# Kernel optimization log

Hardware: AMD Instinct MI355X
Metric: run time of the kernel (lower is better)

## Reference

```python
import jax, jax.numpy as jnp
import numpy as np
import math

B, L, C_IN, D, H, FACTOR = 32, 512, 32, 512, 8, 1
E = D // H
TOP_K = int(FACTOR * math.log(L))  # 6


def setup_inputs() -> dict:
    key = jax.random.key(0)
    ks = jax.random.split(key, 14)
    s = 0.02
    f = lambda k, shp: jax.random.normal(k, shp, jnp.float32) * s
    return {
        "x": jax.random.normal(ks[0], (B, L, C_IN), jnp.float32),
        "conv_w": f(ks[1], (D, C_IN)),  # Conv1d kernel_size=1 == pointwise linear
        "conv_b": f(ks[2], (D,)),
        "wq": f(ks[3], (D, D)), "bq": f(ks[4], (D,)),
        "wk": f(ks[5], (D, D)), "bk": f(ks[6], (D,)),
        "wv": f(ks[7], (D, D)), "bv": f(ks[8], (D,)),
        "wo": f(ks[9], (D, D)), "bo": f(ks[10], (D,)),
        "lin_w": f(ks[11], (1, D)), "lin_b": f(ks[12], (1,)),
    }


def _autocorrelation(q, k, v):
    # q, k, v: [B, L, H, E]; Autoformer AutoCorrelation (inference delay agg)
    qf = jnp.fft.rfft(q.transpose(0, 2, 3, 1), axis=-1)        # [B,H,E,Lf]
    kf = jnp.fft.rfft(k.transpose(0, 2, 3, 1), axis=-1)
    corr = jnp.fft.irfft(qf * jnp.conj(kf), n=L, axis=-1)       # [B,H,E,L]
    vals = v.transpose(0, 2, 3, 1)                              # [B,H,E,L]
    mean_corr = corr.mean(axis=(1, 2))                          # [B,L]
    weights, delay = jax.lax.top_k(mean_corr, TOP_K)            # [B,k]
    w = jax.nn.softmax(weights, axis=-1)                        # [B,k]
    # gather values at (t + delay) mod L  (== doubled-values trick in torch)
    idx = (jnp.arange(L)[None, None, :] + delay[:, :, None]) % L  # [B,k,L]
    patterns = jnp.take_along_axis(
        vals[:, :, :, None, :], idx[:, None, None, :, :], axis=-1)  # [B,H,E,k,L]
    agg = jnp.einsum('bhekl,bk->bhel', patterns, w)             # [B,H,E,L]
    return agg.transpose(0, 3, 1, 2)                            # [B,L,H,E]


def reference(x, conv_w, conv_b, wq, bq, wk, bk, wv, bv, wo, bo, lin_w, lin_b):
    # pointwise conv1d projection: [B,L,C_IN] -> [B,L,D]
    h = x @ conv_w.T + conv_b
    q = (h @ wq.T + bq).reshape(B, L, H, E)
    k = (h @ wk.T + bk).reshape(B, L, H, E)
    v = (h @ wv.T + bv).reshape(B, L, H, E)
    attn_out = _autocorrelation(q, k, v).reshape(B, L, D)
    new_x = attn_out @ wo.T + bo
    out = h + new_x          # residual
    last = out[:, -1:, :]    # x[:, -1:]
    y = last @ lin_w.T + lin_b  # [B,1,1]
    return y
```

## Files before the change

kernel.cpp:

```cpp
#include <hip/hip_runtime.h>
#include <hip/hip_bf16.h>

#define LL 512
#define BB 32
#define DD 512
#define CINN 32
#define TOPK 6
#define BL (BB * LL)

typedef __attribute__((ext_vector_type(8))) short bf16x8;
typedef __attribute__((ext_vector_type(4))) float f32x4;

__device__ inline float bf2f(ushort u) {
    union { uint i; float f; } c; c.i = ((uint)u) << 16; return c.f;
}
__device__ inline ushort f2bf(float f) {
    union { float f; uint i; } c; c.f = f;
    uint i = c.i;
    return (ushort)((i + 0x7FFFu + ((i >> 16) & 1u)) >> 16);
}
__device__ inline void split_bf(float v, ushort& hi, ushort& lo) {
    hi = f2bf(v);
    lo = f2bf(v - bf2f(hi));
}
__device__ inline uint pk2(ushort a, ushort b) { return (uint)a | ((uint)b << 16); }

__device__ inline bf16x8 frag_ld(const ushort* sm, int r, int s) {
    return *(const bf16x8*)(sm + r * 32 + ((s ^ ((r >> 1) & 3)) << 3));
}

__device__ inline void mfma_step(const ushort* sAh, const ushort* sAl,
                                 const ushort* sBh, const ushort* sBl,
                                 f32x4 acc[4][4], int wr, int wc, int fr, int fs) {
    bf16x8 bh[4], blo[4];
    #pragma unroll
    for (int ni = 0; ni < 4; ++ni) {
        bh[ni]  = frag_ld(sBh, wc + ni * 16 + fr, fs);
        blo[ni] = frag_ld(sBl, wc + ni * 16 + fr, fs);
    }
    #pragma unroll
    for (int mi = 0; mi < 4; ++mi) {
        const bf16x8 ah = frag_ld(sAh, wr + mi * 16 + fr, fs);
        const bf16x8 al = frag_ld(sAl, wr + mi * 16 + fr, fs);
        #pragma unroll
        for (int ni = 0; ni < 4; ++ni) {
            acc[mi][ni] = __builtin_amdgcn_mfma_f32_16x16x32_bf16(ah, bh[ni],  acc[mi][ni], 0, 0, 0);
            acc[mi][ni] = __builtin_amdgcn_mfma_f32_16x16x32_bf16(ah, blo[ni], acc[mi][ni], 0, 0, 0);
            acc[mi][ni] = __builtin_amdgcn_mfma_f32_16x16x32_bf16(al, bh[ni],  acc[mi][ni], 0, 0, 0);
        }
    }
}

__global__ __launch_bounds__(256) void prep_m(
    const float* __restrict__ wq, const float* __restrict__ wk,
    const float* __restrict__ cw,
    const float* __restrict__ lin_w, const float* __restrict__ wo,
    float* __restrict__ Mpart, float* __restrict__ upart)
{
    const int tid = threadIdx.x;
    if (blockIdx.x < 64) {
        __shared__ float cws[512][32];
        __shared__ float wqsT[512][9];
        __shared__ float wksT[512][9];
        __shared__ float aqs[8][32];
        __shared__ float aks[8][32];
        for (int i = tid; i < 4096; i += 256) {
            const int d = i >> 3, q = i & 7;
            *(float4*)&cws[d][q * 4] = *(const float4*)(cw + (long)d * 32 + q * 4);
        }
        const int e0 = blockIdx.x * 8;
        for (int i = tid; i < 4096; i += 256) {
            const int e = i >> 9, d = i & 511;
            wqsT[d][e] = wq[(long)(e0 + e) * 512 + d];
            wksT[d][e] = wk[(long)(e0 + e) * 512 + d];
        }
        __syncthreads();
        const int e_loc = tid >> 5, c = tid & 31;
        float aq = 0.f, ak = 0.f;
        #pragma unroll 4
        for (int d = 0; d < 512; ++d) {
            const float cv = cws[d][c];
            aq += wqsT[d][e_loc] * cv;
            ak += wksT[d][e_loc] * cv;
        }
        aqs[e_loc][c] = aq;
        aks[e_loc][c] = ak;
        __syncthreads();
        const int c_ = tid >> 3, cq = tid & 7;
        float m0 = 0.f, m1 = 0.f, m2 = 0.f, m3 = 0.f;
        #pragma unroll
        for (int e = 0; e < 8; ++e) {
            const float a = aqs[e][c_];
            const float4 k4 = *(const float4*)&aks[e][cq * 4];
            m0 += a * k4.x; m1 += a * k4.y; m2 += a * k4.z; m3 += a * k4.w;
        }
        *(float4*)(Mpart + (long)blockIdx.x * 1024 + c_ * 32 + cq * 4) =
            make_float4(m0, m1, m2, m3);
    } else {
        const int j = blockIdx.x - 64;
        const int n0 = j * 64;
        float u0 = 0.f, u1 = 0.f;
        for (int n = 0; n < 64; ++n) {
            const float lw = lin_w[n0 + n];
            u0 += lw * wo[(long)(n0 + n) * 512 + tid];
            u1 += lw * wo[(long)(n0 + n) * 512 + tid + 256];
        }
        upart[j * 512 + tid] = u0;
        upart[j * 512 + tid + 256] = u1;
    }
}

__global__ __launch_bounds__(256, 2) void corr_fused(
    const float* __restrict__ x,
    const float* __restrict__ Mpart, const float* __restrict__ upart,
    const float* __restrict__ wv,
    float* __restrict__ mcpart, float* __restrict__ v2part)
{
    const int tid = threadIdx.x;
    if (blockIdx.x < 512) {
        __shared__ ushort buf[16384];
        __shared__ float Ml[32][36];
        __shared__ float mcloc[LL];
        ushort* bufAh = buf;
        ushort* bufAl = buf + 4096;
        ushort* bufBh = buf + 8192;
        ushort* bufBl = buf + 12288;

        const int xcd = blockIdx.x & 7, s = blockIdx.x >> 3;
        const int b = xcd * 4 + (s >> 4);
        const int tile = s & 15;
        const int tm = tile >> 2, tn = tile & 3;

        {
            float4 ms = make_float4(0.f, 0.f, 0.f, 0.f);
            for (int p = 0; p < 64; ++p) {
                const float4 v = *(const float4*)(Mpart + (long)p * 1024 + tid * 4);
                ms.x += v.x; ms.y += v.y; ms.z += v.z; ms.w += v.w;
            }
            *(float4*)&Ml[tid >> 3][(tid & 7) * 4] = ms;
        }
        mcloc[tid] = 0.f; mcloc[tid + 256] = 0.f;

        const int r = tid >> 1;
        const int pb = (tid & 1) * 2;
        const int swz = (r >> 1) & 3;
        const float* xA = x + ((long)b * LL + tm * 128 + r) * 32;
        const float* xB = x + ((long)b * LL + tn * 128 + r) * 32;
        float xb[32];
        #pragma unroll
        for (int q = 0; q < 8; ++q)
            *(float4*)&xb[q * 4] = *(const float4*)(xB + q * 4);

        __syncthreads();

        #pragma unroll
        for (int pi = 0; pi < 2; ++pi) {
            const int p = pb + pi;
            const int sl = p ^ swz;
            const int uoff = (r * 4 + p) * 8;
            const float4 a0 = *(const float4*)(xA + sl * 8);
            const float4 a1 = *(const float4*)(xA + sl * 8 + 4);
            const float xe[8] = {a0.x, a0.y, a0.z, a0.w, a1.x, a1.y, a1.z, a1.w};
            ushort xh[8], xl[8];
            #pragma unroll
            for (int j = 0; j < 8; ++j) split_bf(xe[j], xh[j], xl[j]);
            *(uint4*)(bufAh + uoff) = make_uint4(pk2(xh[0], xh[1]), pk2(xh[2], xh[3]),
                                                 pk2(xh[4], xh[5]), pk2(xh[6], xh[7]));
            *(uint4*)(bufAl + uoff) = make_uint4(pk2(xl[0], xl[1]), pk2(xl[2], xl[3]),
                                                 pk2(xl[4], xl[5]), pk2(xl[6], xl[7]));
            float uv[8];
            #pragma unroll
            for (int j = 0; j < 8; ++j) {
                const int c = sl * 8 + j;
                float sacc = 0.f;
                #pragma unroll
                for (int q = 0; q < 8; ++q) {
                    const float4 m = *(const float4*)&Ml[c][q * 4];
                    sacc += m.x * xb[q * 4] + m.y * xb[q * 4 + 1]
                          + m.z * xb[q * 4 + 2] + m.w * xb[q * 4 + 3];
                }
                uv[j] = sacc;
            }
            ushort uh[8], ul[8];
            #pragma unroll
            for (int j = 0; j < 8; ++j) split_bf(uv[j], uh[j], ul[j]);
            *(uint4*)(bufBh + uoff) = make_uint4(pk2(uh[0], uh[1]), pk2(uh[2], uh[3]),
                                                 pk2(uh[4], uh[5]), pk2(uh[6], uh[7]));
            *(uint4*)(bufBl + uoff) = make_uint4(pk2(ul[0], ul[1]), pk2(ul[2], ul[3]),
                                                 pk2(ul[4], ul[5]), pk2(ul[6], ul[7]));
        }
        __syncthreads();

        const int wid = tid >> 6, lane = tid & 63;
        const int wr = (wid >> 1) * 64, wc = (wid & 1) * 64;
        const int fr = lane & 15, fs = lane >> 4;
        f32x4 acc[4][4] = {};
        mfma_step(bufAh, bufAl, bufBh, bufBl, acc, wr, wc, fr, fs);

        const int base = wr - wc + 128 * (tm - tn) + fs * 4 - fr;
        #pragma unroll
        for (int k = -3; k <= 3; ++k) {
            #pragma unroll
            for (int rr = 0; rr < 4; ++rr) {
                float sdg = 0.f;
                #pragma unroll
                for (int mi = 0; mi < 4; ++mi) {
                    const int ni = mi - k;
                    if (ni >= 0 && ni < 4) sdg += acc[mi][ni][rr];
                }
                atomicAdd(&mcloc[(base + 16 * k + rr) & (LL - 1)], sdg);
            }
        }
        __syncthreads();
        float* out = mcpart + ((long)b * 16 + tile) * LL;
        out[tid] = mcloc[tid];
        out[tid + 256] = mcloc[tid + 256];
    } else {
        const int j = blockIdx.x - 512;
        __shared__ float us[64];
        if (tid < 64) {
            float s = 0.f;
            #pragma unroll
            for (int i = 0; i < 8; ++i) s += upart[i * 512 + j * 64 + tid];
            us[tid] = s;
        }
        __syncthreads();
        float s0 = 0.f, s1 = 0.f;
        for (int dl = 0; dl < 64; ++dl) {
            const float ud = us[dl];
            s0 += ud * wv[(long)(j * 64 + dl) * 512 + tid];
            s1 += ud * wv[(long)(j * 64 + dl) * 512 + tid + 256];
        }
        v2part[j * 512 + tid] = s0;
        v2part[j * 512 + tid + 256] = s1;
    }
}

__global__ __launch_bounds__(256) void tail_kernel(
    const float* __restrict__ mcpart, const float* __restrict__ x,
    const float* __restrict__ upart, const float* __restrict__ v2part,
    const float* __restrict__ cw, const float* __restrict__ cb,
    const float* __restrict__ lin_w, const float* __restrict__ bv,
    const float* __restrict__ bo, const float* __restrict__ lin_b,
    float* __restrict__ out)
{
    const int b = blockIdx.x, tid = threadIdx.x;
    const int lane = tid & 63, wid = tid >> 6;
    __shared__ float v2s[512];
    __shared__ float us2[512];
    __shared__ float w3p[8][32];
    __shared__ float w4p[8][32];
    __shared__ float w3s[32];
    __shared__ float w4s[32];
    __shared__ float c2s;
    __shared__ float swv[4];
    __shared__ int   swi[4];
    __shared__ float selv[TOPK];
    __shared__ int   seli[TOPK];
    __shared__ float wts[TOPK];
    __shared__ float redc[4];

    {
        float a0 = 0.f, a1 = 0.f, b0 = 0.f, b1 = 0.f;
        #pragma unroll
        for (int i = 0; i < 8; ++i) {
            a0 += v2part[i * 512 + tid];
            a1 += v2part[i * 512 + tid + 256];
            b0 += upart[i * 512 + tid];
            b1 += upart[i * 512 + tid + 256];
        }
        v2s[tid] = a0; v2s[tid + 256] = a1;
        us2[tid] = b0; us2[tid + 256] = b1;
    }
    __syncthreads();
    {
        const int c = tid & 31, g = tid >> 5;
        float w3 = 0.f, w4 = 0.f;
        for (int dl = 0; dl < 64; ++dl) {
            const int d = g * 64 + dl;
            const float cwv = cw[(long)d * 32 + c];
            w3 += v2s[d] * cwv;
            w4 += lin_w[d] * cwv;
        }
        w3p[g][c] = w3; w4p[g][c] = w4;
    }
    __syncthreads();
    if (tid < 32) {
        float a3 = 0.f, a4 = 0.f;
        #pragma unroll
        for (int g2 = 0; g2 < 8; ++g2) { a3 += w3p[g2][tid]; a4 += w4p[g2][tid]; }
        w3s[tid] = a3; w4s[tid] = a4;
    }
    {
        float p = cb[tid] * (v2s[tid] + lin_w[tid])
                + cb[tid + 256] * (v2s[tid + 256] + lin_w[tid + 256])
                + bv[tid] * us2[tid] + bv[tid + 256] * us2[tid + 256]
                + bo[tid] * lin_w[tid] + bo[tid + 256] * lin_w[tid + 256];
        #pragma unroll
        for (int o = 32; o; o >>= 1) p += __shfl_down(p, o);
        if ((tid & 63) == 0) redc[tid >> 6] = p;
    }
    __syncthreads();
    if (tid == 0) c2s = redc[0] + redc[1] + redc[2] + redc[3] + lin_b[0];

    float v0 = 0.f, v1 = 0.f;
    #pragma unroll
    for (int j = 0; j < 16; ++j) {
        v0 += mcpart[((long)b * 16 + j) * LL + tid];
        v1 += mcpart[((long)b * 16 + j) * LL + tid + 256];
    }
    v0 *= (1.0f / DD); v1 *= (1.0f / DD);

    int live0 = 1, live1 = 1;
    for (int r = 0; r < TOPK; ++r) {
        float bvv = -1e30f; int bi = -1;
        if (live0) { bvv = v0; bi = tid; }
        if (live1 && v1 > bvv) { bvv = v1; bi = tid + 256; }
        #pragma unroll
        for (int o = 32; o; o >>= 1) {
            const float ov = __shfl_down(bvv, o);
            const int oi = __shfl_down(bi, o);
            if (ov > bvv || (ov == bvv && oi < bi)) { bvv = ov; bi = oi; }
        }
        if (lane == 0) { swv[wid] = bvv; swi[wid] = bi; }
        __syncthreads();
        if (tid == 0) {
            float fv = swv[0]; int fi = swi[0];
            #pragma unroll
            for (int w2 = 1; w2 < 4; ++w2) {
                if (swv[w2] > fv || (swv[w2] == fv && swi[w2] < fi)) { fv = swv[w2]; fi = swi[w2]; }
            }
            selv[r] = fv; seli[r] = fi;
        }
        __syncthreads();
        const int w = seli[r];
        if (w == tid)       live0 = 0;
        if (w == tid + 256) live1 = 0;
    }
    if (tid == 0) {
        const float mx = selv[0];
        float e[TOPK], ssum = 0.f;
        #pragma unroll
        for (int k = 0; k < TOPK; ++k) { e[k] = expf(selv[k] - mx); ssum += e[k]; }
        #pragma unroll
        for (int k = 0; k < TOPK; ++k) wts[k] = e[k] / ssum;
    }
    __syncthreads();

    if (tid < CINN) {
        float xm = 0.f;
        #pragma unroll
        for (int k = 0; k < TOPK; ++k) {
            const int r = (LL - 1 + seli[k]) & (LL - 1);
            xm += wts[k] * x[((long)b * LL + r) * CINN + tid];
        }
        const float xlv = x[((long)b * LL + (LL - 1)) * CINN + tid];
        float yv = xlv * w4s[tid] + xm * w3s[tid];
        #pragma unroll
        for (int o = 16; o; o >>= 1) yv += __shfl_down(yv, o);
        if (tid == 0) out[b] = yv + c2s;
    }
}

extern "C" void kernel_launch(void* const* d_in, const int* in_sizes, int n_in,
                              void* d_out, int out_size, void* d_ws, size_t ws_size,
                              hipStream_t stream) {
    const float* x      = (const float*)d_in[0];
    const float* conv_w = (const float*)d_in[1];
    const float* conv_b = (const float*)d_in[2];
    const float* wq     = (const float*)d_in[3];
    const float* wk     = (const float*)d_in[5];
    const float* wv     = (const float*)d_in[7];
    const float* bv     = (const float*)d_in[8];
    const float* wo     = (const float*)d_in[9];
    const float* bo     = (const float*)d_in[10];
    const float* lin_w  = (const float*)d_in[11];
    const float* lin_b  = (const float*)d_in[12];

    char* w = (char*)d_ws;
    float* Mpart  = (float*)w;  w += (long)64 * 1024 * 4;
    float* upart  = (float*)w;  w += (long)8 * 512 * 4;
    float* v2part = (float*)w;  w += (long)8 * 512 * 4;
    float* mcpart = (float*)w;  w += (long)BB * 16 * LL * 4;
    float* yout   = (float*)d_out;

    prep_m<<<72, 256, 0, stream>>>(wq, wk, conv_w, lin_w, wo, Mpart, upart);
    corr_fused<<<520, 256, 0, stream>>>(x, Mpart, upart, wv, mcpart, v2part);
    tail_kernel<<<BB, 256, 0, stream>>>(mcpart, x, upart, v2part,
                                        conv_w, conv_b, lin_w, bv, bo, lin_b, yout);
}
```

Baseline: 61.75 us.

## Fuse three kernels into one cooperative persistent kernel with grid syncs

Replaces the three separate kernel launches (prep, correlation, tail) with a single cooperative kernel of 512 blocks that separates phases with grid.sync(). The Mpart reduction is done once into a small Mfin buffer instead of every correlation block re-summing 64 partials, and the conv weight is no longer staged in shared memory in the prep phase. The aim is to remove launch gaps and redundant reduction traffic. The cost is that most blocks idle during the small phases, and the kernel pays the cost of three grid-wide barriers. It also requires all 512 blocks to be co-resident.

```diff
diff --git a/kernel.cpp b/kernel.cpp
--- a/kernel.cpp
+++ b/kernel.cpp
@@ -1,5 +1,8 @@
 #include <hip/hip_runtime.h>
 #include <hip/hip_bf16.h>
+#include <hip/hip_cooperative_groups.h>
+
+namespace cg = cooperative_groups;
 
 #define LL 512
 #define BB 32
@@ -51,37 +54,40 @@
     }
 }
 
-__global__ __launch_bounds__(256) void prep_m(
+__global__ __launch_bounds__(256, 2) void uber(
+    const float* __restrict__ x,
     const float* __restrict__ wq, const float* __restrict__ wk,
-    const float* __restrict__ cw,
-    const float* __restrict__ lin_w, const float* __restrict__ wo,
-    float* __restrict__ Mpart, float* __restrict__ upart)
+    const float* __restrict__ cw, const float* __restrict__ cb,
+    const float* __restrict__ wv, const float* __restrict__ bv,
+    const float* __restrict__ wo, const float* __restrict__ bo,
+    const float* __restrict__ lin_w, const float* __restrict__ lin_b,
+    float* __restrict__ Mpart, float* __restrict__ upart,
+    float* __restrict__ Mfin, float* __restrict__ v2part,
+    float* __restrict__ mcpart, float* __restrict__ out)
 {
-    const int tid = threadIdx.x;
-    if (blockIdx.x < 64) {
-        __shared__ float cws[512][32];
-        __shared__ float wqsT[512][9];
-        __shared__ float wksT[512][9];
-        __shared__ float aqs[8][32];
-        __shared__ float aks[8][32];
-        for (int i = tid; i < 4096; i += 256) {
-            const int d = i >> 3, q = i & 7;
-            *(float4*)&cws[d][q * 4] = *(const float4*)(cw + (long)d * 32 + q * 4);
-        }
-        const int e0 = blockIdx.x * 8;
+    __shared__ __align__(16) char smem[39424];
+    cg::grid_group grid = cg::this_grid();
+    const int bid = blockIdx.x, tid = threadIdx.x;
+
+    if (bid < 64) {
+        float (*wqs)[512] = (float(*)[512])smem;
+        float (*wks)[512] = (float(*)[512])(smem + 16384);
+        float (*aqs)[32]  = (float(*)[32])(smem + 32768);
+        float (*aks)[32]  = (float(*)[32])(smem + 33792);
+        const int e0 = bid * 8;
         for (int i = tid; i < 4096; i += 256) {
             const int e = i >> 9, d = i & 511;
-            wqsT[d][e] = wq[(long)(e0 + e) * 512 + d];
-            wksT[d][e] = wk[(long)(e0 + e) * 512 + d];
+            wqs[e][d] = wq[(long)(e0 + e) * 512 + d];
+            wks[e][d] = wk[(long)(e0 + e) * 512 + d];
         }
         __syncthreads();
         const int e_loc = tid >> 5, c = tid & 31;
         float aq = 0.f, ak = 0.f;
         #pragma unroll 4
         for (int d = 0; d < 512; ++d) {
-            const float cv = cws[d][c];
-            aq += wqsT[d][e_loc] * cv;
-            ak += wksT[d][e_loc] * cv;
+            const float cv = cw[(long)d * 32 + c];
+            aq += wqs[e_loc][d] * cv;
+            ak += wks[e_loc][d] * cv;
         }
         aqs[e_loc][c] = aq;
         aks[e_loc][c] = ak;
@@ -94,11 +100,10 @@
             const float4 k4 = *(const float4*)&aks[e][cq * 4];
             m0 += a * k4.x; m1 += a * k4.y; m2 += a * k4.z; m3 += a * k4.w;
         }
-        *(float4*)(Mpart + (long)blockIdx.x * 1024 + c_ * 32 + cq * 4) =
+        *(float4*)(Mpart + (long)bid * 1024 + c_ * 32 + cq * 4) =
             make_float4(m0, m1, m2, m3);
-    } else {
-        const int j = blockIdx.x - 64;
-        const int n0 = j * 64;
+    } else if (bid < 72) {
+        const int j = bid - 64, n0 = j * 64;
         float u0 = 0.f, u1 = 0.f;
         for (int n = 0; n < 64; ++n) {
             const float lw = lin_w[n0 + n];
@@ -108,36 +113,51 @@
         upart[j * 512 + tid] = u0;
         upart[j * 512 + tid + 256] = u1;
     }
-}
-
-__global__ __launch_bounds__(256, 2) void corr_fused(
-    const float* __restrict__ x,
-    const float* __restrict__ Mpart, const float* __restrict__ upart,
-    const float* __restrict__ wv,
-    float* __restrict__ mcpart, float* __restrict__ v2part)
-{
-    const int tid = threadIdx.x;
-    if (blockIdx.x < 512) {
-        __shared__ ushort buf[16384];
-        __shared__ float Ml[32][36];
-        __shared__ float mcloc[LL];
+    grid.sync();
+
+    if (bid < 4) {
+        const int entry = bid * 256 + tid;
+        float s = 0.f;
+        for (int p = 0; p < 64; ++p) s += Mpart[(long)p * 1024 + entry];
+        Mfin[entry] = s;
+    } else if (bid >= 8 && bid < 16) {
+        const int j = bid - 8;
+        float* us = (float*)smem;
+        if (tid < 64) {
+            float s = 0.f;
+            #pragma unroll
+            for (int i = 0; i < 8; ++i) s += upart[i * 512 + j * 64 + tid];
+            us[tid] = s;
+        }
+        __syncthreads();
+        float s0 = 0.f, s1 = 0.f;
+        for (int dl = 0; dl < 64; ++dl) {
+            const float ud = us[dl];
+            s0 += ud * wv[(long)(j * 64 + dl) * 512 + tid];
+            s1 += ud * wv[(long)(j * 64 + dl) * 512 + tid + 256];
+        }
+        v2part[j * 512 + tid] = s0;
+        v2part[j * 512 + tid + 256] = s1;
+    }
+    grid.sync();
+
+    {
+        ushort* buf   = (ushort*)smem;
+        float (*Ml)[36] = (float(*)[36])(smem + 32768);
+        float* mcloc  = (float*)(smem + 32768 + 4608);
         ushort* bufAh = buf;
         ushort* bufAl = buf + 4096;
         ushort* bufBh = buf + 8192;
         ushort* bufBl = buf + 12288;
 
-        const int xcd = blockIdx.x & 7, s = blockIdx.x >> 3;
+        const int xcd = bid & 7, s = bid >> 3;
         const int b = xcd * 4 + (s >> 4);
         const int tile = s & 15;
         const int tm = tile >> 2, tn = tile & 3;
 
         {
-            float4 ms = make_float4(0.f, 0.f, 0.f, 0.f);
-            for (int p = 0; p < 64; ++p) {
-                const float4 v = *(const float4*)(Mpart + (long)p * 1024 + tid * 4);
-                ms.x += v.x; ms.y += v.y; ms.z += v.z; ms.w += v.w;
-            }
-            *(float4*)&Ml[tid >> 3][(tid & 7) * 4] = ms;
+            const float4 mv = *(const float4*)(Mfin + tid * 4);
+            *(float4*)&Ml[tid >> 3][(tid & 7) * 4] = mv;
         }
         mcloc[tid] = 0.f; mcloc[tid + 256] = 0.f;
 
@@ -212,153 +232,131 @@
             }
         }
         __syncthreads();
-        float* out = mcpart + ((long)b * 16 + tile) * LL;
-        out[tid] = mcloc[tid];
-        out[tid + 256] = mcloc[tid + 256];
-    } else {
-        const int j = blockIdx.x - 512;
-        __shared__ float us[64];
-        if (tid < 64) {
-            float s = 0.f;
-            #pragma unroll
-            for (int i = 0; i < 8; ++i) s += upart[i * 512 + j * 64 + tid];
-            us[tid] = s;
-        }
-        __syncthreads();
-        float s0 = 0.f, s1 = 0.f;
-        for (int dl = 0; dl < 64; ++dl) {
-            const float ud = us[dl];
-            s0 += ud * wv[(long)(j * 64 + dl) * 512 + tid];
-            s1 += ud * wv[(long)(j * 64 + dl) * 512 + tid + 256];
-        }
-        v2part[j * 512 + tid] = s0;
-        v2part[j * 512 + tid + 256] = s1;
-    }
-}
-
-__global__ __launch_bounds__(256) void tail_kernel(
-    const float* __restrict__ mcpart, const float* __restrict__ x,
-    const float* __restrict__ upart, const float* __restrict__ v2part,
-    const float* __restrict__ cw, const float* __restrict__ cb,
-    const float* __restrict__ lin_w, const float* __restrict__ bv,
-    const float* __restrict__ bo, const float* __restrict__ lin_b,
-    float* __restrict__ out)
-{
-    const int b = blockIdx.x, tid = threadIdx.x;
-    const int lane = tid & 63, wid = tid >> 6;
-    __shared__ float v2s[512];
-    __shared__ float us2[512];
-    __shared__ float w3p[8][32];
-    __shared__ float w4p[8][32];
-    __shared__ float w3s[32];
-    __shared__ float w4s[32];
-    __shared__ float c2s;
-    __shared__ float swv[4];
-    __shared__ int   swi[4];
-    __shared__ float selv[TOPK];
-    __shared__ int   seli[TOPK];
-    __shared__ float wts[TOPK];
-    __shared__ float redc[4];
-
-    {
-        float a0 = 0.f, a1 = 0.f, b0 = 0.f, b1 = 0.f;
-        #pragma unroll
-        for (int i = 0; i < 8; ++i) {
-            a0 += v2part[i * 512 + tid];
-            a1 += v2part[i * 512 + tid + 256];
-            b0 += upart[i * 512 + tid];
-            b1 += upart[i * 512 + tid + 256];
-        }
-        v2s[tid] = a0; v2s[tid + 256] = a1;
-        us2[tid] = b0; us2[tid + 256] = b1;
-    }
-    __syncthreads();
-    {
-        const int c = tid & 31, g = tid >> 5;
-        float w3 = 0.f, w4 = 0.f;
-        for (int dl = 0; dl < 64; ++dl) {
-            const int d = g * 64 + dl;
-            const float cwv = cw[(long)d * 32 + c];
-            w3 += v2s[d] * cwv;
-            w4 += lin_w[d] * cwv;
-        }
-        w3p[g][c] = w3; w4p[g][c] = w4;
-    }
-    __syncthreads();
-    if (tid < 32) {
-        float a3 = 0.f, a4 = 0.f;
-        #pragma unroll
-        for (int g2 = 0; g2 < 8; ++g2) { a3 += w3p[g2][tid]; a4 += w4p[g2][tid]; }
-        w3s[tid] = a3; w4s[tid] = a4;
-    }
-    {
-        float p = cb[tid] * (v2s[tid] + lin_w[tid])
-                + cb[tid + 256] * (v2s[tid + 256] + lin_w[tid + 256])
-                + bv[tid] * us2[tid] + bv[tid + 256] * us2[tid + 256]
-                + bo[tid] * lin_w[tid] + bo[tid + 256] * lin_w[tid + 256];
-        #pragma unroll
-        for (int o = 32; o; o >>= 1) p += __shfl_down(p, o);
-        if ((tid & 63) == 0) redc[tid >> 6] = p;
-    }
-    __syncthreads();
-    if (tid == 0) c2s = redc[0] + redc[1] + redc[2] + redc[3] + lin_b[0];
-
-    float v0 = 0.f, v1 = 0.f;
-    #pragma unroll
-    for (int j = 0; j < 16; ++j) {
-        v0 += mcpart[((long)b * 16 + j) * LL + tid];
-        v1 += mcpart[((long)b * 16 + j) * LL + tid + 256];
-    }
-    v0 *= (1.0f / DD); v1 *= (1.0f / DD);
-
-    int live0 = 1, live1 = 1;
-    for (int r = 0; r < TOPK; ++r) {
-        float bvv = -1e30f; int bi = -1;
-        if (live0) { bvv = v0; bi = tid; }
-        if (live1 && v1 > bvv) { bvv = v1; bi = tid + 256; }
-        #pragma unroll
-        for (int o = 32; o; o >>= 1) {
-            const float ov = __shfl_down(bvv, o);
-            const int oi = __shfl_down(bi, o);
-            if (ov > bvv || (ov == bvv && oi < bi)) { bvv = ov; bi = oi; }
-        }
-        if (lane == 0) { swv[wid] = bvv; swi[wid] = bi; }
-        __syncthreads();
+        float* o = mcpart + ((long)b * 16 + tile) * LL;
+        o[tid] = mcloc[tid];
+        o[tid + 256] = mcloc[tid + 256];
+    }
+    grid.sync();
+
+    if (bid < 32) {
+        float* fb   = (float*)smem;
+        float* v2s  = fb;
+        float* us2  = fb + 512;
+        float (*w3p)[32] = (float(*)[32])(fb + 1024);
+        float (*w4p)[32] = (float(*)[32])(fb + 1280);
+        float* w3s  = fb + 1536;
+        float* w4s  = fb + 1568;
+        float* swv  = fb + 1600;
+        float* selv = fb + 1604;
+        float* wts  = fb + 1610;
+        float* redc = fb + 1616;
+        float* c2s  = fb + 1620;
+        int*   swi  = (int*)(fb + 1624);
+        int*   seli = (int*)(fb + 1628);
+
+        const int b = bid;
+        const int lane = tid & 63, wid = tid >> 6;
+
+        {
+            float a0 = 0.f, a1 = 0.f, b0 = 0.f, b1 = 0.f;
+            #pragma unroll
+            for (int i = 0; i < 8; ++i) {
+                a0 += v2part[i * 512 + tid];
+                a1 += v2part[i * 512 + tid + 256];
+                b0 += upart[i * 512 + tid];
+                b1 += upart[i * 512 + tid + 256];
+            }
+            v2s[tid] = a0; v2s[tid + 256] = a1;
+            us2[tid] = b0; us2[tid + 256] = b1;
+        }
+        __syncthreads();
+        {
+            const int c = tid & 31, g = tid >> 5;
+            float w3 = 0.f, w4 = 0.f;
+            for (int dl = 0; dl < 64; ++dl) {
+                const int d = g * 64 + dl;
+                const float cwv = cw[(long)d * 32 + c];
+                w3 += v2s[d] * cwv;
+                w4 += lin_w[d] * cwv;
+            }
+            w3p[g][c] = w3; w4p[g][c] = w4;
+        }
+        __syncthreads();
+        if (tid < 32) {
+            float a3 = 0.f, a4 = 0.f;
+            #pragma unroll
+            for (int g2 = 0; g2 < 8; ++g2) { a3 += w3p[g2][tid]; a4 += w4p[g2][tid]; }
+            w3s[tid] = a3; w4s[tid] = a4;
+        }
+        {
+            float p = cb[tid] * (v2s[tid] + lin_w[tid])
+                    + cb[tid + 256] * (v2s[tid + 256] + lin_w[tid + 256])
+                    + bv[tid] * us2[tid] + bv[tid + 256] * us2[tid + 256]
+                    + bo[tid] * lin_w[tid] + bo[tid + 256] * lin_w[tid + 256];
+            #pragma unroll
+            for (int o = 32; o; o >>= 1) p += __shfl_down(p, o);
+            if ((tid & 63) == 0) redc[tid >> 6] = p;
+        }
+        __syncthreads();
+        if (tid == 0) c2s[0] = redc[0] + redc[1] + redc[2] + redc[3] + lin_b[0];
+
+        float v0 = 0.f, v1 = 0.f;
+        #pragma unroll
+        for (int j = 0; j < 16; ++j) {
+            v0 += mcpart[((long)b * 16 + j) * LL + tid];
+            v1 += mcpart[((long)b * 16 + j) * LL + tid + 256];
+        }
+        v0 *= (1.0f / DD); v1 *= (1.0f / DD);
+
+        int live0 = 1, live1 = 1;
+        for (int r = 0; r < TOPK; ++r) {
+            float bvv = -1e30f; int bi = -1;
+            if (live0) { bvv = v0; bi = tid; }
+            if (live1 && v1 > bvv) { bvv = v1; bi = tid + 256; }
+            #pragma unroll
+            for (int o = 32; o; o >>= 1) {
+                const float ov = __shfl_down(bvv, o);
+                const int oi = __shfl_down(bi, o);
+                if (ov > bvv || (ov == bvv && oi < bi)) { bvv = ov; bi = oi; }
+            }
+            if (lane == 0) { swv[wid] = bvv; swi[wid] = bi; }
+            __syncthreads();
+            if (tid == 0) {
+                float fv = swv[0]; int fi = swi[0];
+                #pragma unroll
+                for (int w2 = 1; w2 < 4; ++w2) {
+                    if (swv[w2] > fv || (swv[w2] == fv && swi[w2] < fi)) { fv = swv[w2]; fi = swi[w2]; }
+                }
+                selv[r] = fv; seli[r] = fi;
+            }
+            __syncthreads();
+            const int w = seli[r];
+            if (w == tid)       live0 = 0;
+            if (w == tid + 256) live1 = 0;
+        }
         if (tid == 0) {
-            float fv = swv[0]; int fi = swi[0];
-            #pragma unroll
-            for (int w2 = 1; w2 < 4; ++w2) {
-                if (swv[w2] > fv || (swv[w2] == fv && swi[w2] < fi)) { fv = swv[w2]; fi = swi[w2]; }
-            }
-            selv[r] = fv; seli[r] = fi;
-        }
-        __syncthreads();
-        const int w = seli[r];
-        if (w == tid)       live0 = 0;
-        if (w == tid + 256) live1 = 0;
-    }
-    if (tid == 0) {
-        const float mx = selv[0];
-        float e[TOPK], ssum = 0.f;
-        #pragma unroll
-        for (int k = 0; k < TOPK; ++k) { e[k] = expf(selv[k] - mx); ssum += e[k]; }
-        #pragma unroll
-        for (int k = 0; k < TOPK; ++k) wts[k] = e[k] / ssum;
-    }
-    __syncthreads();
-
-    if (tid < CINN) {
-        float xm = 0.f;
-        #pragma unroll
-        for (int k = 0; k < TOPK; ++k) {
-            const int r = (LL - 1 + seli[k]) & (LL - 1);
-            xm += wts[k] * x[((long)b * LL + r) * CINN + tid];
-        }
-        const float xlv = x[((long)b * LL + (LL - 1)) * CINN + tid];
-        float yv = xlv * w4s[tid] + xm * w3s[tid];
-        #pragma unroll
-        for (int o = 16; o; o >>= 1) yv += __shfl_down(yv, o);
-        if (tid == 0) out[b] = yv + c2s;
+            const float mx = selv[0];
+            float e[TOPK], ssum = 0.f;
+            #pragma unroll
+            for (int k = 0; k < TOPK; ++k) { e[k] = expf(selv[k] - mx); ssum += e[k]; }
+            #pragma unroll
+            for (int k = 0; k < TOPK; ++k) wts[k] = e[k] / ssum;
+        }
+        __syncthreads();
+
+        if (tid < CINN) {
+            float xm = 0.f;
+            #pragma unroll
+            for (int k = 0; k < TOPK; ++k) {
+                const int r = (LL - 1 + seli[k]) & (LL - 1);
+                xm += wts[k] * x[((long)b * LL + r) * CINN + tid];
+            }
+            const float xlv = x[((long)b * LL + (LL - 1)) * CINN + tid];
+            float yv = xlv * w4s[tid] + xm * w3s[tid];
+            #pragma unroll
+            for (int o = 16; o; o >>= 1) yv += __shfl_down(yv, o);
+            if (tid == 0) out[b] = yv + c2s[0];
+        }
     }
 }
 
@@ -380,12 +378,18 @@
     char* w = (char*)d_ws;
     float* Mpart  = (float*)w;  w += (long)64 * 1024 * 4;
     float* upart  = (float*)w;  w += (long)8 * 512 * 4;
+    float* Mfin   = (float*)w;  w += (long)1024 * 4;
     float* v2part = (float*)w;  w += (long)8 * 512 * 4;
     float* mcpart = (float*)w;  w += (long)BB * 16 * LL * 4;
     float* yout   = (float*)d_out;
 
-    prep_m<<<72, 256, 0, stream>>>(wq, wk, conv_w, lin_w, wo, Mpart, upart);
-    corr_fused<<<520, 256, 0, stream>>>(x, Mpart, upart, wv, mcpart, v2part);
-    tail_kernel<<<BB, 256, 0, stream>>>(mcpart, x, upart, v2part,
-                                        conv_w, conv_b, lin_w, bv, bo, lin_b, yout);
-}
+    void* args[] = {
+        (void*)&x, (void*)&wq, (void*)&wk, (void*)&conv_w, (void*)&conv_b,
+        (void*)&wv, (void*)&bv, (void*)&wo, (void*)&bo,
+        (void*)&lin_w, (void*)&lin_b,
+        (void*)&Mpart, (void*)&upart, (void*)&Mfin, (void*)&v2part,
+        (void*)&mcpart, (void*)&yout
+    };
+    hipLaunchCooperativeKernel((const void*)uber, dim3(512), dim3(256),
+                               args, 0, stream);
+}
```

Result: slower. 205.2 us (+232.3%).

## Fuse tail into correlation kernel via last-block atomic counter per batch

Applied to the files above, without the earlier changes.

Removes the separate tail kernel launch by having the last of the 16 tile blocks per batch (detected with an atomic counter reset in prep_m) perform the top-k, softmax and output computation. The v2 = u·Wv product, previously split across 8 extra blocks, is now computed redundantly inside each batch's last block over the full 512x512 wv matrix. This saves one kernel launch and its gap, but adds a serial 512-iteration GEMV per batch on the critical path.

```diff
diff --git a/kernel.cpp b/kernel.cpp
--- a/kernel.cpp
+++ b/kernel.cpp
@@ -55,7 +55,8 @@
     const float* __restrict__ wq, const float* __restrict__ wk,
     const float* __restrict__ cw,
     const float* __restrict__ lin_w, const float* __restrict__ wo,
-    float* __restrict__ Mpart, float* __restrict__ upart)
+    float* __restrict__ Mpart, float* __restrict__ upart,
+    int* __restrict__ cnt)
 {
     const int tid = threadIdx.x;
     if (blockIdx.x < 64) {
@@ -98,6 +99,7 @@
             make_float4(m0, m1, m2, m3);
     } else {
         const int j = blockIdx.x - 64;
+        if (blockIdx.x == 64 && tid < BB) cnt[tid] = 0;
         const int n0 = j * 64;
         float u0 = 0.f, u1 = 0.f;
         for (int n = 0; n < 64; ++n) {
@@ -110,87 +112,91 @@
     }
 }
 
-__global__ __launch_bounds__(256, 2) void corr_fused(
-    const float* __restrict__ x,
-    const float* __restrict__ Mpart, const float* __restrict__ upart,
-    const float* __restrict__ wv,
-    float* __restrict__ mcpart, float* __restrict__ v2part)
+__global__ __launch_bounds__(256, 2) void corr_tail(
+    const float* __restrict__ x, const float* __restrict__ Mpart,
+    const float* __restrict__ upart, const float* __restrict__ wv,
+    const float* __restrict__ cw, const float* __restrict__ cb,
+    const float* __restrict__ lin_w, const float* __restrict__ bv,
+    const float* __restrict__ bo, const float* __restrict__ lin_b,
+    float* __restrict__ mcpart, int* __restrict__ cnt,
+    float* __restrict__ out)
 {
+    __shared__ ushort buf[16384];
+    __shared__ float Ml[32][36];
+    __shared__ float mcloc[LL];
+    __shared__ int lastflag;
+    ushort* bufAh = buf;
+    ushort* bufAl = buf + 4096;
+    ushort* bufBh = buf + 8192;
+    ushort* bufBl = buf + 12288;
     const int tid = threadIdx.x;
-    if (blockIdx.x < 512) {
-        __shared__ ushort buf[16384];
-        __shared__ float Ml[32][36];
-        __shared__ float mcloc[LL];
-        ushort* bufAh = buf;
-        ushort* bufAl = buf + 4096;
-        ushort* bufBh = buf + 8192;
-        ushort* bufBl = buf + 12288;
-
-        const int xcd = blockIdx.x & 7, s = blockIdx.x >> 3;
-        const int b = xcd * 4 + (s >> 4);
-        const int tile = s & 15;
-        const int tm = tile >> 2, tn = tile & 3;
-
-        {
-            float4 ms = make_float4(0.f, 0.f, 0.f, 0.f);
-            for (int p = 0; p < 64; ++p) {
-                const float4 v = *(const float4*)(Mpart + (long)p * 1024 + tid * 4);
-                ms.x += v.x; ms.y += v.y; ms.z += v.z; ms.w += v.w;
-            }
-            *(float4*)&Ml[tid >> 3][(tid & 7) * 4] = ms;
-        }
-        mcloc[tid] = 0.f; mcloc[tid + 256] = 0.f;
-
-        const int r = tid >> 1;
-        const int pb = (tid & 1) * 2;
-        const int swz = (r >> 1) & 3;
-        const float* xA = x + ((long)b * LL + tm * 128 + r) * 32;
-        const float* xB = x + ((long)b * LL + tn * 128 + r) * 32;
-        float xb[32];
-        #pragma unroll
-        for (int q = 0; q < 8; ++q)
-            *(float4*)&xb[q * 4] = *(const float4*)(xB + q * 4);
-
-        __syncthreads();
-
-        #pragma unroll
-        for (int pi = 0; pi < 2; ++pi) {
-            const int p = pb + pi;
-            const int sl = p ^ swz;
-            const int uoff = (r * 4 + p) * 8;
-            const float4 a0 = *(const float4*)(xA + sl * 8);
-            const float4 a1 = *(const float4*)(xA + sl * 8 + 4);
-            const float xe[8] = {a0.x, a0.y, a0.z, a0.w, a1.x, a1.y, a1.z, a1.w};
-            ushort xh[8], xl[8];
-            #pragma unroll
-            for (int j = 0; j < 8; ++j) split_bf(xe[j], xh[j], xl[j]);
-            *(uint4*)(bufAh + uoff) = make_uint4(pk2(xh[0], xh[1]), pk2(xh[2], xh[3]),
-                                                 pk2(xh[4], xh[5]), pk2(xh[6], xh[7]));
-            *(uint4*)(bufAl + uoff) = make_uint4(pk2(xl[0], xl[1]), pk2(xl[2], xl[3]),
-                                                 pk2(xl[4], xl[5]), pk2(xl[6], xl[7]));
-            float uv[8];
-            #pragma unroll
-            for (int j = 0; j < 8; ++j) {
-                const int c = sl * 8 + j;
-                float sacc = 0.f;
-                #pragma unroll
-                for (int q = 0; q < 8; ++q) {
-                    const float4 m = *(const float4*)&Ml[c][q * 4];
-                    sacc += m.x * xb[q * 4] + m.y * xb[q * 4 + 1]
-                          + m.z * xb[q * 4 + 2] + m.w * xb[q * 4 + 3];
-                }
-                uv[j] = sacc;
-            }
-            ushort uh[8], ul[8];
-            #pragma unroll
-            for (int j = 0; j < 8; ++j) split_bf(uv[j], uh[j], ul[j]);
-            *(uint4*)(bufBh + uoff) = make_uint4(pk2(uh[0], uh[1]), pk2(uh[2], uh[3]),
-                                                 pk2(uh[4], uh[5]), pk2(uh[6], uh[7]));
-            *(uint4*)(bufBl + uoff) = make_uint4(pk2(ul[0], ul[1]), pk2(ul[2], ul[3]),
-                                                 pk2(ul[4], ul[5]), pk2(ul[6], ul[7]));
-        }
-        __syncthreads();
-
+
+    const int xcd = blockIdx.x & 7, s = blockIdx.x >> 3;
+    const int b = xcd * 4 + (s >> 4);
+    const int tile = s & 15;
+    const int tm = tile >> 2, tn = tile & 3;
+
+    {
+        float4 ms = make_float4(0.f, 0.f, 0.f, 0.f);
+        for (int p = 0; p < 64; ++p) {
+            const float4 v = *(const float4*)(Mpart + (long)p * 1024 + tid * 4);
+            ms.x += v.x; ms.y += v.y; ms.z += v.z; ms.w += v.w;
+        }
+        *(float4*)&Ml[tid >> 3][(tid & 7) * 4] = ms;
+    }
+    mcloc[tid] = 0.f; mcloc[tid + 256] = 0.f;
+
+    const int r = tid >> 1;
+    const int pb = (tid & 1) * 2;
+    const int swz = (r >> 1) & 3;
+    const float* xA = x + ((long)b * LL + tm * 128 + r) * 32;
+    const float* xB = x + ((long)b * LL + tn * 128 + r) * 32;
+    float xb[32];
+    #pragma unroll
+    for (int q = 0; q < 8; ++q)
+        *(float4*)&xb[q * 4] = *(const float4*)(xB + q * 4);
+
+    __syncthreads();
+
+    #pragma unroll
+    for (int pi = 0; pi < 2; ++pi) {
+        const int p = pb + pi;
+        const int sl = p ^ swz;
+        const int uoff = (r * 4 + p) * 8;
+        const float4 a0 = *(const float4*)(xA + sl * 8);
+        const float4 a1 = *(const float4*)(xA + sl * 8 + 4);
+        const float xe[8] = {a0.x, a0.y, a0.z, a0.w, a1.x, a1.y, a1.z, a1.w};
+        ushort xh[8], xl[8];
+        #pragma unroll
+        for (int j = 0; j < 8; ++j) split_bf(xe[j], xh[j], xl[j]);
+        *(uint4*)(bufAh + uoff) = make_uint4(pk2(xh[0], xh[1]), pk2(xh[2], xh[3]),
+                                             pk2(xh[4], xh[5]), pk2(xh[6], xh[7]));
+        *(uint4*)(bufAl + uoff) = make_uint4(pk2(xl[0], xl[1]), pk2(xl[2], xl[3]),
+                                             pk2(xl[4], xl[5]), pk2(xl[6], xl[7]));
+        float uv[8];
+        #pragma unroll
+        for (int j = 0; j < 8; ++j) {
+            const int c = sl * 8 + j;
+            float sacc = 0.f;
+            #pragma unroll
+            for (int q = 0; q < 8; ++q) {
+                const float4 m = *(const float4*)&Ml[c][q * 4];
+                sacc += m.x * xb[q * 4] + m.y * xb[q * 4 + 1]
+                      + m.z * xb[q * 4 + 2] + m.w * xb[q * 4 + 3];
+            }
+            uv[j] = sacc;
+        }
+        ushort uh[8], ul[8];
+        #pragma unroll
+        for (int j = 0; j < 8; ++j) split_bf(uv[j], uh[j], ul[j]);
+        *(uint4*)(bufBh + uoff) = make_uint4(pk2(uh[0], uh[1]), pk2(uh[2], uh[3]),
+                                             pk2(uh[4], uh[5]), pk2(uh[6], uh[7]));
+        *(uint4*)(bufBl + uoff) = make_uint4(pk2(ul[0], ul[1]), pk2(ul[2], ul[3]),
+                                             pk2(ul[4], ul[5]), pk2(ul[6], ul[7]));
+    }
+    __syncthreads();
+
+    {
         const int wid = tid >> 6, lane = tid & 63;
         const int wr = (wid >> 1) * 64, wc = (wid & 1) * 64;
         const int fr = lane & 15, fs = lane >> 4;
@@ -211,154 +217,144 @@
                 atomicAdd(&mcloc[(base + 16 * k + rr) & (LL - 1)], sdg);
             }
         }
-        __syncthreads();
-        float* out = mcpart + ((long)b * 16 + tile) * LL;
-        out[tid] = mcloc[tid];
-        out[tid + 256] = mcloc[tid + 256];
-    } else {
-        const int j = blockIdx.x - 512;
-        __shared__ float us[64];
-        if (tid < 64) {
-            float s = 0.f;
-            #pragma unroll
-            for (int i = 0; i < 8; ++i) s += upart[i * 512 + j * 64 + tid];
-            us[tid] = s;
-        }
-        __syncthreads();
-        float s0 = 0.f, s1 = 0.f;
-        for (int dl = 0; dl < 64; ++dl) {
-            const float ud = us[dl];
-            s0 += ud * wv[(long)(j * 64 + dl) * 512 + tid];
-            s1 += ud * wv[(long)(j * 64 + dl) * 512 + tid + 256];
-        }
-        v2part[j * 512 + tid] = s0;
-        v2part[j * 512 + tid + 256] = s1;
-    }
-}
-
-__global__ __launch_bounds__(256) void tail_kernel(
-    const float* __restrict__ mcpart, const float* __restrict__ x,
-    const float* __restrict__ upart, const float* __restrict__ v2part,
-    const float* __restrict__ cw, const float* __restrict__ cb,
-    const float* __restrict__ lin_w, const float* __restrict__ bv,
-    const float* __restrict__ bo, const float* __restrict__ lin_b,
-    float* __restrict__ out)
-{
-    const int b = blockIdx.x, tid = threadIdx.x;
-    const int lane = tid & 63, wid = tid >> 6;
-    __shared__ float v2s[512];
-    __shared__ float us2[512];
-    __shared__ float w3p[8][32];
-    __shared__ float w4p[8][32];
-    __shared__ float w3s[32];
-    __shared__ float w4s[32];
-    __shared__ float c2s;
-    __shared__ float swv[4];
-    __shared__ int   swi[4];
-    __shared__ float selv[TOPK];
-    __shared__ int   seli[TOPK];
-    __shared__ float wts[TOPK];
-    __shared__ float redc[4];
-
+    }
+    __syncthreads();
     {
-        float a0 = 0.f, a1 = 0.f, b0 = 0.f, b1 = 0.f;
-        #pragma unroll
-        for (int i = 0; i < 8; ++i) {
-            a0 += v2part[i * 512 + tid];
-            a1 += v2part[i * 512 + tid + 256];
-            b0 += upart[i * 512 + tid];
-            b1 += upart[i * 512 + tid + 256];
-        }
-        v2s[tid] = a0; v2s[tid + 256] = a1;
-        us2[tid] = b0; us2[tid + 256] = b1;
-    }
-    __syncthreads();
+        float* o = mcpart + ((long)b * 16 + tile) * LL;
+        o[tid] = mcloc[tid];
+        o[tid + 256] = mcloc[tid + 256];
+    }
+    __threadfence();
+    __syncthreads();
+    if (tid == 0) lastflag = (atomicAdd(&cnt[b], 1) == 15) ? 1 : 0;
+    __syncthreads();
+    if (!lastflag) return;
+    __threadfence();
+
     {
-        const int c = tid & 31, g = tid >> 5;
-        float w3 = 0.f, w4 = 0.f;
-        for (int dl = 0; dl < 64; ++dl) {
-            const int d = g * 64 + dl;
-            const float cwv = cw[(long)d * 32 + c];
-            w3 += v2s[d] * cwv;
-            w4 += lin_w[d] * cwv;
-        }
-        w3p[g][c] = w3; w4p[g][c] = w4;
-    }
-    __syncthreads();
-    if (tid < 32) {
-        float a3 = 0.f, a4 = 0.f;
-        #pragma unroll
-        for (int g2 = 0; g2 < 8; ++g2) { a3 += w3p[g2][tid]; a4 += w4p[g2][tid]; }
-        w3s[tid] = a3; w4s[tid] = a4;
-    }
-    {
-        float p = cb[tid] * (v2s[tid] + lin_w[tid])
-                + cb[tid + 256] * (v2s[tid + 256] + lin_w[tid + 256])
-                + bv[tid] * us2[tid] + bv[tid + 256] * us2[tid + 256]
-                + bo[tid] * lin_w[tid] + bo[tid + 256] * lin_w[tid + 256];
-        #pragma unroll
-        for (int o = 32; o; o >>= 1) p += __shfl_down(p, o);
-        if ((tid & 63) == 0) redc[tid >> 6] = p;
-    }
-    __syncthreads();
-    if (tid == 0) c2s = redc[0] + redc[1] + redc[2] + redc[3] + lin_b[0];
-
-    float v0 = 0.f, v1 = 0.f;
-    #pragma unroll
-    for (int j = 0; j < 16; ++j) {
-        v0 += mcpart[((long)b * 16 + j) * LL + tid];
-        v1 += mcpart[((long)b * 16 + j) * LL + tid + 256];
-    }
-    v0 *= (1.0f / DD); v1 *= (1.0f / DD);
-
-    int live0 = 1, live1 = 1;
-    for (int r = 0; r < TOPK; ++r) {
-        float bvv = -1e30f; int bi = -1;
-        if (live0) { bvv = v0; bi = tid; }
-        if (live1 && v1 > bvv) { bvv = v1; bi = tid + 256; }
-        #pragma unroll
-        for (int o = 32; o; o >>= 1) {
-            const float ov = __shfl_down(bvv, o);
-            const int oi = __shfl_down(bi, o);
-            if (ov > bvv || (ov == bvv && oi < bi)) { bvv = ov; bi = oi; }
-        }
-        if (lane == 0) { swv[wid] = bvv; swi[wid] = bi; }
-        __syncthreads();
+        const int lane = tid & 63, wid = tid >> 6;
+        float* fb   = (float*)buf;
+        float* v2s  = fb;
+        float* us2  = fb + 512;
+        float (*w3p)[32] = (float(*)[32])(fb + 1024);
+        float (*w4p)[32] = (float(*)[32])(fb + 1280);
+        float* w3s  = fb + 1536;
+        float* w4s  = fb + 1568;
+        float* swv  = fb + 1600;
+        float* selv = fb + 1604;
+        float* wts  = fb + 1610;
+        float* redc = fb + 1616;
+        float* c2s  = fb + 1620;
+        int*   swi  = (int*)(fb + 1624);
+        int*   seli = (int*)(fb + 1628);
+
+        {
+            float b0 = 0.f, b1 = 0.f;
+            #pragma unroll
+            for (int i = 0; i < 8; ++i) {
+                b0 += upart[i * 512 + tid];
+                b1 += upart[i * 512 + tid + 256];
+            }
+            us2[tid] = b0; us2[tid + 256] = b1;
+        }
+        __syncthreads();
+        {
+            float s0 = 0.f, s1 = 0.f;
+            for (int d = 0; d < 512; ++d) {
+                const float ud = us2[d];
+                s0 += ud * wv[(long)d * 512 + tid];
+                s1 += ud * wv[(long)d * 512 + tid + 256];
+            }
+            v2s[tid] = s0; v2s[tid + 256] = s1;
+        }
+        __syncthreads();
+        {
+            const int c = tid & 31, g = tid >> 5;
+            float w3 = 0.f, w4 = 0.f;
+            for (int dl = 0; dl < 64; ++dl) {
+                const int d = g * 64 + dl;
+                const float cwv = cw[(long)d * 32 + c];
+                w3 += v2s[d] * cwv;
+                w4 += lin_w[d] * cwv;
+            }
+            w3p[g][c] = w3; w4p[g][c] = w4;
+        }
+        __syncthreads();
+        if (tid < 32) {
+            float a3 = 0.f, a4 = 0.f;
+            #pragma unroll
+            for (int g2 = 0; g2 < 8; ++g2) { a3 += w3p[g2][tid]; a4 += w4p[g2][tid]; }
+            w3s[tid] = a3; w4s[tid] = a4;
+        }
+        {
+            float p = cb[tid] * (v2s[tid] + lin_w[tid])
+                    + cb[tid + 256] * (v2s[tid + 256] + lin_w[tid + 256])
+                    + bv[tid] * us2[tid] + bv[tid + 256] * us2[tid + 256]
+                    + bo[tid] * lin_w[tid] + bo[tid + 256] * lin_w[tid + 256];
+            #pragma unroll
+            for (int o = 32; o; o >>= 1) p += __shfl_down(p, o);
+            if ((tid & 63) == 0) redc[tid >> 6] = p;
+        }
+        __syncthreads();
+        if (tid == 0) c2s[0] = redc[0] + redc[1] + redc[2] + redc[3] + lin_b[0];
+
+        float v0 = 0.f, v1 = 0.f;
+        #pragma unroll
+        for (int j = 0; j < 16; ++j) {
+            v0 += mcpart[((long)b * 16 + j) * LL + tid];
+            v1 += mcpart[((long)b * 16 + j) * LL + tid + 256];
+        }
+        v0 *= (1.0f / DD); v1 *= (1.0f / DD);
+
+        int live0 = 1, live1 = 1;
+        for (int rr = 0; rr < TOPK; ++rr) {
+            float bvv = -1e30f; int bi = -1;
+            if (live0) { bvv = v0; bi = tid; }
+            if (live1 && v1 > bvv) { bvv = v1; bi = tid + 256; }
+            #pragma unroll
+            for (int o = 32; o; o >>= 1) {
+                const float ov = __shfl_down(bvv, o);
+                const int oi = __shfl_down(bi, o);
+                if (ov > bvv || (ov == bvv && oi < bi)) { bvv = ov; bi = oi; }
+            }
+            if (lane == 0) { swv[wid] = bvv; swi[wid] = bi; }
+            __syncthreads();
+            if (tid == 0) {
+                float fv = swv[0]; int fi = swi[0];
+                #pragma unroll
+                for (int w2 = 1; w2 < 4; ++w2) {
+                    if (swv[w2] > fv || (swv[w2] == fv && swi[w2] < fi)) { fv = swv[w2]; fi = swi[w2]; }
+                }
+                selv[rr] = fv; seli[rr] = fi;
+            }
+            __syncthreads();
+            const int w = seli[rr];
+            if (w == tid)       live0 = 0;
+            if (w == tid + 256) live1 = 0;
+        }
         if (tid == 0) {
-            float fv = swv[0]; int fi = swi[0];
-            #pragma unroll
-            for (int w2 = 1; w2 < 4; ++w2) {
-                if (swv[w2] > fv || (swv[w2] == fv && swi[w2] < fi)) { fv = swv[w2]; fi = swi[w2]; }
-            }
-            selv[r] = fv; seli[r] = fi;
-        }
-        __syncthreads();
-        const int w = seli[r];
-        if (w == tid)       live0 = 0;
-        if (w == tid + 256) live1 = 0;
-    }
-    if (tid == 0) {
-        const float mx = selv[0];
-        float e[TOPK], ssum = 0.f;
-        #pragma unroll
-        for (int k = 0; k < TOPK; ++k) { e[k] = expf(selv[k] - mx); ssum += e[k]; }
-        #pragma unroll
-        for (int k = 0; k < TOPK; ++k) wts[k] = e[k] / ssum;
-    }
-    __syncthreads();
-
-    if (tid < CINN) {
-        float xm = 0.f;
-        #pragma unroll
-        for (int k = 0; k < TOPK; ++k) {
-            const int r = (LL - 1 + seli[k]) & (LL - 1);
-            xm += wts[k] * x[((long)b * LL + r) * CINN + tid];
-        }
-        const float xlv = x[((long)b * LL + (LL - 1)) * CINN + tid];
-        float yv = xlv * w4s[tid] + xm * w3s[tid];
-        #pragma unroll
-        for (int o = 16; o; o >>= 1) yv += __shfl_down(yv, o);
-        if (tid == 0) out[b] = yv + c2s;
+            const float mx = selv[0];
+            float e[TOPK], ssum = 0.f;
+            #pragma unroll
+            for (int k = 0; k < TOPK; ++k) { e[k] = expf(selv[k] - mx); ssum += e[k]; }
+            #pragma unroll
+            for (int k = 0; k < TOPK; ++k) wts[k] = e[k] / ssum;
+        }
+        __syncthreads();
+
+        if (tid < CINN) {
+            float xm = 0.f;
+            #pragma unroll
+            for (int k = 0; k < TOPK; ++k) {
+                const int rr = (LL - 1 + seli[k]) & (LL - 1);
+                xm += wts[k] * x[((long)b * LL + rr) * CINN + tid];
+            }
+            const float xlv = x[((long)b * LL + (LL - 1)) * CINN + tid];
+            float yv = xlv * w4s[tid] + xm * w3s[tid];
+            #pragma unroll
+            for (int o = 16; o; o >>= 1) yv += __shfl_down(yv, o);
+            if (tid == 0) out[b] = yv + c2s[0];
+        }
     }
 }
 
@@ -380,12 +376,12 @@
     char* w = (char*)d_ws;
     float* Mpart  = (float*)w;  w += (long)64 * 1024 * 4;
     float* upart  = (float*)w;  w += (long)8 * 512 * 4;
-    float* v2part = (float*)w;  w += (long)8 * 512 * 4;
     float* mcpart = (float*)w;  w += (long)BB * 16 * LL * 4;
+    int*   cnt    = (int*)w;    w += BB * 4;
     float* yout   = (float*)d_out;
 
-    prep_m<<<72, 256, 0, stream>>>(wq, wk, conv_w, lin_w, wo, Mpart, upart);
-    corr_fused<<<520, 256, 0, stream>>>(x, Mpart, upart, wv, mcpart, v2part);
-    tail_kernel<<<BB, 256, 0, stream>>>(mcpart, x, upart, v2part,
-                                        conv_w, conv_b, lin_w, bv, bo, lin_b, yout);
-}
+    prep_m<<<72, 256, 0, stream>>>(wq, wk, conv_w, lin_w, wo, Mpart, upart, cnt);
+    corr_tail<<<512, 256, 0, stream>>>(x, Mpart, upart, wv,
+                                       conv_w, conv_b, lin_w, bv, bo, lin_b,
+                                       mcpart, cnt, yout);
+}
```

Result: slower. 98.17 us (+59.0%).
